# Kernel tuning notes

Measured on AMD Instinct MI355X. Metric: run time of the kernel, lower is better.

The kernel has to match this reference:

```python
import jax, jax.numpy as jnp
import numpy as np

N_ATOMS = 65536
N_SPECIES = 4
N_MOL = 512
F_PS = 512
F_MP = 256
H = 256
EPS = 1e-5


def _layer_norm(x, gamma, beta):
    mu = jnp.mean(x, axis=-1, keepdims=True)
    var = jnp.mean(jnp.square(x - mu), axis=-1, keepdims=True)
    return (x - mu) * jax.lax.rsqrt(var + EPS) * gamma + beta


def _species_mlp(x, W1, W2, W3):
    # x: [N, F], atoms grouped into S contiguous equal-size species blocks.
    S = W1.shape[0]
    N, F = x.shape
    xs = x.reshape(S, N // S, F)                       # [S, N/S, F]
    h = jax.nn.silu(jnp.einsum('snf,sfh->snh', xs, W1))  # grouped GEMM + SiLU
    h = jax.nn.silu(jnp.einsum('snh,sho->sno', h, W2))
    e = jnp.einsum('snh,sho->sno', h, W3)              # [S, N/S, 1]
    return e.reshape(N, -1)                            # keys_to_samples: back to per-atom


def setup_inputs() -> dict:
    key = jax.random.key(0)
    ks = jax.random.split(key, 10)
    inp = {
        'x_ps': jax.random.normal(ks[0], (N_ATOMS, F_PS), dtype=jnp.float32),
        'x_mp': jax.random.normal(ks[1], (N_ATOMS, F_MP), dtype=jnp.float32),
        'batch': jax.random.randint(ks[2], (N_ATOMS,), 0, N_MOL),
        'gamma_ps': jnp.ones((F_PS,), jnp.float32),
        'beta_ps': jnp.zeros((F_PS,), jnp.float32),
        'gamma_mp': jnp.ones((F_MP,), jnp.float32),
        'beta_mp': jnp.zeros((F_MP,), jnp.float32),
        'W_ps1': jax.random.normal(ks[3], (N_SPECIES, F_PS, H), jnp.float32) / np.sqrt(F_PS),
        'W_ps2': jax.random.normal(ks[4], (N_SPECIES, H, H), jnp.float32) / np.sqrt(H),
        'W_ps3': jax.random.normal(ks[5], (N_SPECIES, H, 1), jnp.float32) / np.sqrt(H),
        'W_mp1': jax.random.normal(ks[6], (N_SPECIES, F_MP, H), jnp.float32) / np.sqrt(F_MP),
        'W_mp2': jax.random.normal(ks[7], (N_SPECIES, H, H), jnp.float32) / np.sqrt(H),
        'W_mp3': jax.random.normal(ks[8], (N_SPECIES, H, 1), jnp.float32) / np.sqrt(H),
    }
    return inp


def reference(x_ps, x_mp, batch, gamma_ps, beta_ps, gamma_mp, beta_mp,
              W_ps1, W_ps2, W_ps3, W_mp1, W_mp2, W_mp3):
    norm_factor = jnp.float32(1.0)  # normalization_factor buffer
    f_ps = _layer_norm(x_ps, gamma_ps, beta_ps)
    f_mp = _layer_norm(x_mp, gamma_mp, beta_mp)
    e_ps = _species_mlp(f_ps, W_ps1, W_ps2, W_ps3)   # [N, 1] per-atom energies
    e_mp = _species_mlp(f_mp, W_mp1, W_mp2, W_mp3)   # [N, 1]
    # index_add_ scatter: per-atom -> per-molecule
    energies_ps = jax.ops.segment_sum(e_ps, batch, num_segments=N_MOL) / norm_factor
    energies_mp = jax.ops.segment_sum(e_mp, batch, num_segments=N_MOL) / norm_factor
    return energies_ps + energies_mp                 # [N_MOL, 1] (training path)
```

## Files before the change

kernel.cpp:

```cpp
#include <hip/hip_runtime.h>
#include <hip/hip_bf16.h>

#define N_ATOMS 65536
#define N_MOL 512

typedef __attribute__((ext_vector_type(8))) __bf16 bf16x8;
typedef __attribute__((ext_vector_type(4))) float f32x4;

__device__ __forceinline__ unsigned int f2bf(float f) {
    unsigned int u = __float_as_uint(f);
    return (u + 0x7fffu + ((u >> 16) & 1u)) >> 16;
}

__device__ __forceinline__ int pack2n(float a, float b) {
    union { __hip_bfloat162 h; int u; } c;
    c.h = __float22bfloat162_rn(make_float2(a, b));
    return c.u;
}

__device__ __forceinline__ short bf1(float a) {
    union { __hip_bfloat16 h; short s; } c;
    c.h = __float2bfloat16(a);
    return c.s;
}

__device__ __forceinline__ float silu(float v) {
    return v / (1.0f + __expf(-v));
}

#define GLDS16(gp, lp)                                                        \
    __builtin_amdgcn_global_load_lds(                                         \
        (__attribute__((address_space(1))) void*)(uintptr_t)(gp),             \
        (__attribute__((address_space(3))) void*)(uintptr_t)(lp), 16, 0, 0)

#define WS_W1PS 0
#define WS_W2PS 524288
#define WS_W1MP 786432
#define WS_W2MP 1048576
#define WS_GB_BYTES 2621440

__global__ __launch_bounds__(256) void prep_w(const float* __restrict__ Wps1,
                                              const float* __restrict__ Wps2,
                                              const float* __restrict__ Wmp1,
                                              const float* __restrict__ Wmp2,
                                              const float* __restrict__ g_ps,
                                              const float* __restrict__ b_ps,
                                              const float* __restrict__ g_mp,
                                              const float* __restrict__ b_mp,
                                              short* __restrict__ wdst,
                                              float* __restrict__ gb) {
    int b = blockIdx.x;
    const float* src; int K; long dstbase; int s, c;
    const float* ga = nullptr; const float* be = nullptr; float* gbd = nullptr;
    if (b < 32)      { src = Wps1; K = 512; s = b >> 3;        c = b & 7;        dstbase = WS_W1PS;
                       ga = g_ps; be = b_ps; gbd = gb; }
    else if (b < 48) { src = Wps2; K = 256; s = (b - 32) >> 2; c = (b - 32) & 3; dstbase = WS_W2PS; }
    else if (b < 64) { src = Wmp1; K = 256; s = (b - 48) >> 2; c = (b - 48) & 3; dstbase = WS_W1MP;
                       ga = g_mp; be = b_mp; gbd = gb + 2048; }
    else             { src = Wmp2; K = 256; s = (b - 64) >> 2; c = (b - 64) & 3; dstbase = WS_W2MP; }
    int n = threadIdx.x;
    int k0 = c * 64;
    const float* sp = src + (long)s * K * 256 + (long)k0 * 256 + n;
    int4* dstc = (int4*)(wdst + dstbase + (long)s * K * 256 + (long)c * 16384);
    float gs = 0.0f, bs = 0.0f;
    #pragma unroll 2
    for (int j = 0; j < 8; ++j) {
        unsigned int hh[8];
        #pragma unroll
        for (int i = 0; i < 8; ++i) {
            int kl = j * 8 + i;
            float v = sp[(long)kl * 256];
            float w = ga ? v * ga[k0 + kl] : v;
            hh[i] = f2bf(w);
            if (ga) {
                gs += __uint_as_float(hh[i] << 16);
                bs += be[k0 + kl] * v;
            }
        }
        int4 p;
        p.x = (int)(hh[0] | (hh[1] << 16));
        p.y = (int)(hh[2] | (hh[3] << 16));
        p.z = (int)(hh[4] | (hh[5] << 16));
        p.w = (int)(hh[6] | (hh[7] << 16));
        int ch = j >> 2;
        int i16 = n * 4 + ((j & 3) ^ ((n >> 1) & 3));
        dstc[ch * 1024 + i16] = p;
    }
    if (ga) {
        atomicAdd(&gbd[s * 256 + n], gs);
        atomicAdd(&gbd[1024 + s * 256 + n], bs);
    }
}

#define OFF_P0    0
#define OFF_AS    32768
#define OFF_H1    16384
#define OFF_STATS 49152
#define OFF_ELDS  49664
#define ARENA_BYTES 49920

#define STAGE_B(gbase, lbase)                                                 \
    do {                                                                      \
        const int4* _g = (const int4*)(gbase);                                \
        int4* _l = (int4*)(lbase);                                            \
        _Pragma("unroll")                                                     \
        for (int _q = 0; _q < 4; ++_q) {                                      \
            int _idx = wid * 256 + _q * 64;                                   \
            GLDS16(_g + _idx + lane, _l + _idx);                              \
        }                                                                     \
    } while (0)

template <int NPH>
__device__ __forceinline__ void mlp_body(
    char* arena,
    const float* __restrict__ x, const short* __restrict__ W1,
    const short* __restrict__ W2, const float* __restrict__ gW1,
    const float* __restrict__ bW1, const float* __restrict__ W3,
    const int* __restrict__ batch, float* __restrict__ out, int tile) {
    short* P0  = (short*)(arena + OFF_P0);
    short* As  = (short*)(arena + OFF_AS);
    short* H1  = (short*)(arena + OFF_H1);
    float2* rowstats = (float2*)(arena + OFF_STATS);
    float*  e_lds    = (float*)(arena + OFF_ELDS);

    const int tid = threadIdx.x;
    const int lane = tid & 63;
    const int wid = tid >> 6;
    const int wn = wid * 64;
    const int lg = lane >> 4;
    const int ln = lane & 15;
    const int swz = lg ^ ((ln >> 1) & 3);

    constexpr int F = NPH * 64;
    const int block0 = tile * 64;
    const int species = block0 >> 14;
    const short* W1s = W1 + (size_t)species * NPH * 16384;
    const short* W2s = W2 + (size_t)species * 65536;

    if (tid < 64) e_lds[tid] = 0.0f;
    const int mol = (tid < 64) ? batch[block0 + tid] : 0;

    float gwv[4], bwv[4], w3v[4];
    #pragma unroll
    for (int n = 0; n < 4; ++n) {
        int col = wn + n * 16 + ln;
        gwv[n] = gW1[species * 256 + col];
        bwv[n] = bW1[species * 256 + col];
        w3v[n] = W3[species * 256 + col];
    }

    const int ar = tid >> 2;
    const int aj = tid & 3;
    const float* xrow = x + (size_t)(block0 + ar) * F + aj * 8;
    const int i16a = ar * 4 + (aj ^ ((ar >> 1) & 3));

    f32x4 acc[4][4];
    #pragma unroll
    for (int m = 0; m < 4; ++m)
        #pragma unroll
        for (int n = 0; n < 4; ++n) acc[m][n] = (f32x4){0.f, 0.f, 0.f, 0.f};
    float s1 = 0.0f, s2 = 0.0f;

    float4 cu0 = *(const float4*)(xrow);
    float4 cv0 = *(const float4*)(xrow + 4);
    float4 cu1 = *(const float4*)(xrow + 32);
    float4 cv1 = *(const float4*)(xrow + 36);

    #pragma unroll 1
    for (int p = 0; p < NPH; ++p) {
        if (p) __syncthreads();
        float4 nu0, nv0, nu1, nv1;
        if (p + 1 < NPH) {
            nu0 = *(const float4*)(xrow + (p + 1) * 64);
            nv0 = *(const float4*)(xrow + (p + 1) * 64 + 4);
            nu1 = *(const float4*)(xrow + (p + 1) * 64 + 32);
            nv1 = *(const float4*)(xrow + (p + 1) * 64 + 36);
        }
        STAGE_B(W1s + (size_t)p * 16384, P0);
        STAGE_B(W1s + (size_t)p * 16384 + 8192, P0 + 8192);
        s1 += cu0.x + cu0.y + cu0.z + cu0.w + cv0.x + cv0.y + cv0.z + cv0.w
            + cu1.x + cu1.y + cu1.z + cu1.w + cv1.x + cv1.y + cv1.z + cv1.w;
        s2 += cu0.x * cu0.x + cu0.y * cu0.y + cu0.z * cu0.z + cu0.w * cu0.w
            + cv0.x * cv0.x + cv0.y * cv0.y + cv0.z * cv0.z + cv0.w * cv0.w
            + cu1.x * cu1.x + cu1.y * cu1.y + cu1.z * cu1.z + cu1.w * cu1.w
            + cv1.x * cv1.x + cv1.y * cv1.y + cv1.z * cv1.z + cv1.w * cv1.w;
        {
            int4 q;
            q.x = pack2n(cu0.x, cu0.y); q.y = pack2n(cu0.z, cu0.w);
            q.z = pack2n(cv0.x, cv0.y); q.w = pack2n(cv0.z, cv0.w);
            *(int4*)&As[i16a * 8] = q;
            q.x = pack2n(cu1.x, cu1.y); q.y = pack2n(cu1.z, cu1.w);
            q.z = pack2n(cv1.x, cv1.y); q.w = pack2n(cv1.z, cv1.w);
            *(int4*)&As[2048 + i16a * 8] = q;
        }
        __syncthreads();
        #pragma unroll
        for (int ks = 0; ks < 2; ++ks) {
            bf16x8 a[4], b[4];
            #pragma unroll
            for (int m = 0; m < 4; ++m)
                a[m] = *(const bf16x8*)&As[ks * 2048 + (m * 64 + ln * 4 + swz) * 8];
            #pragma unroll
            for (int n = 0; n < 4; ++n)
                b[n] = *(const bf16x8*)&P0[ks * 8192 + (wn * 4 + n * 64 + ln * 4 + swz) * 8];
            __builtin_amdgcn_s_setprio(1);
            #pragma unroll
            for (int m = 0; m < 4; ++m)
                #pragma unroll
                for (int n = 0; n < 4; ++n)
                    acc[m][n] = __builtin_amdgcn_mfma_f32_16x16x32_bf16(a[m], b[n], acc[m][n], 0, 0, 0);
            __builtin_amdgcn_s_setprio(0);
        }
        if (p + 1 < NPH) { cu0 = nu0; cv0 = nv0; cu1 = nu1; cv1 = nv1; }
    }

    s1 += __shfl_xor(s1, 1); s1 += __shfl_xor(s1, 2);
    s2 += __shfl_xor(s2, 1); s2 += __shfl_xor(s2, 2);
    if (aj == 0) rowstats[ar] = make_float2(s1, s2);
    __syncthreads();

    STAGE_B(W2s, P0);

    const float invF = 1.0f / (float)F;
    #pragma unroll
    for (int m = 0; m < 4; ++m) {
        #pragma unroll
        for (int rr = 0; rr < 4; ++rr) {
            int row = m * 16 + lg * 4 + rr;
            float2 rs = rowstats[row];
            float mu = rs.x * invF;
            float var = rs.y * invF - mu * mu;
            float rstd = rsqrtf(var + 1e-5f);
            float nmu = rstd * mu;
            #pragma unroll
            for (int n = 0; n < 4; ++n) {
                float vv = rstd * acc[m][n][rr] - nmu * gwv[n] + bwv[n];
                int col = wn + n * 16 + ln;
                H1[(row * 256 + col) ^ ((row & 7) << 3)] = bf1(silu(vv));
            }
        }
    }
    __syncthreads();

    f32x4 acc2[4][4];
    #pragma unroll
    for (int m = 0; m < 4; ++m)
        #pragma unroll
        for (int n = 0; n < 4; ++n) acc2[m][n] = (f32x4){0.f, 0.f, 0.f, 0.f};

    #pragma unroll 1
    for (int c = 0; c < 8; ++c) {
        bf16x8 a[4], b[4];
        #pragma unroll
        for (int m = 0; m < 4; ++m)
            a[m] = *(const bf16x8*)&H1[m * 4096 + ln * 256 + ((c * 32 + lg * 8) ^ ((ln & 7) << 3))];
        #pragma unroll
        for (int n = 0; n < 4; ++n)
            b[n] = *(const bf16x8*)&P0[(wn * 4 + n * 64 + ln * 4 + swz) * 8];
        __syncthreads();
        if (c < 7)
            STAGE_B(W2s + (size_t)(c + 1) * 8192, P0);
        __builtin_amdgcn_s_setprio(1);
        #pragma unroll
        for (int m = 0; m < 4; ++m)
            #pragma unroll
            for (int n = 0; n < 4; ++n)
                acc2[m][n] = __builtin_amdgcn_mfma_f32_16x16x32_bf16(a[m], b[n], acc2[m][n], 0, 0, 0);
        __builtin_amdgcn_s_setprio(0);
        __syncthreads();
    }

    #pragma unroll
    for (int m = 0; m < 4; ++m) {
        #pragma unroll
        for (int rr = 0; rr < 4; ++rr) {
            int row = m * 16 + lg * 4 + rr;
            float p = 0.0f;
            #pragma unroll
            for (int n = 0; n < 4; ++n) p += silu(acc2[m][n][rr]) * w3v[n];
            p += __shfl_xor(p, 1); p += __shfl_xor(p, 2);
            p += __shfl_xor(p, 4); p += __shfl_xor(p, 8);
            if (ln == 0) atomicAdd(&e_lds[row], p);
        }
    }
    __syncthreads();
    if (tid < 64) atomicAdd(out + mol, e_lds[tid]);
}

__global__ __launch_bounds__(256, 3) void mlp_all(
    const float* __restrict__ x_ps, const float* __restrict__ x_mp,
    const short* __restrict__ wimg, const float* __restrict__ gb,
    const float* __restrict__ W3ps, const float* __restrict__ W3mp,
    const int* __restrict__ batch, float* __restrict__ out) {
    __shared__ __align__(16) char arena[ARENA_BYTES];
    if (blockIdx.x < 1024) {
        mlp_body<8>(arena, x_ps, wimg + WS_W1PS, wimg + WS_W2PS,
                    gb + 0, gb + 1024, W3ps, batch, out, (int)blockIdx.x);
    } else {
        mlp_body<4>(arena, x_mp, wimg + WS_W1MP, wimg + WS_W2MP,
                    gb + 2048, gb + 3072, W3mp, batch, out, (int)blockIdx.x - 1024);
    }
}

extern "C" void kernel_launch(void* const* d_in, const int* in_sizes, int n_in,
                              void* d_out, int out_size, void* d_ws, size_t ws_size,
                              hipStream_t stream) {
    const float* x_ps     = (const float*)d_in[0];
    const float* x_mp     = (const float*)d_in[1];
    const int*   batch    = (const int*)d_in[2];
    const float* gamma_ps = (const float*)d_in[3];
    const float* beta_ps  = (const float*)d_in[4];
    const float* gamma_mp = (const float*)d_in[5];
    const float* beta_mp  = (const float*)d_in[6];
    const float* W_ps1    = (const float*)d_in[7];
    const float* W_ps2    = (const float*)d_in[8];
    const float* W_ps3    = (const float*)d_in[9];
    const float* W_mp1    = (const float*)d_in[10];
    const float* W_mp2    = (const float*)d_in[11];
    const float* W_mp3    = (const float*)d_in[12];

    float* out = (float*)d_out;
    short* wsW = (short*)d_ws;
    float* gb  = (float*)((char*)d_ws + WS_GB_BYTES);

    hipMemsetAsync(out, 0, N_MOL * sizeof(float), stream);
    hipMemsetAsync(gb, 0, 4096 * sizeof(float), stream);

    hipLaunchKernelGGL(prep_w, dim3(80), dim3(256), 0, stream,
                       W_ps1, W_ps2, W_mp1, W_mp2,
                       gamma_ps, beta_ps, gamma_mp, beta_mp, wsW, gb);

    hipLaunchKernelGGL(mlp_all, dim3(2048), dim3(256), 0, stream,
                       x_ps, x_mp, wsW, gb, W_ps3, W_mp3, batch, out);
}
```

Baseline: 151.0 us.

## Stage fp32 activations directly to LDS and prefetch next phase during MFMA

The input activation tile is now copied straight from global memory into LDS as fp32 with a swizzled layout. Previously it was loaded into registers, converted to bf16 and written to LDS by hand. Each phase reads all of its A and B fragments into registers, syncs, and then issues the next phase's W1 and X loads (or the W2 load on the last phase) before running the MFMAs, so the loads overlap compute. This trades more LDS read traffic, in-register bf16 conversion and larger register pressure for fewer VGPR round-trips and better latency hiding.

```diff
diff --git a/kernel.cpp b/kernel.cpp
--- a/kernel.cpp
+++ b/kernel.cpp
@@ -93,7 +93,7 @@
 }
 
 #define OFF_P0    0
-#define OFF_AS    32768
+#define OFF_XS    32768
 #define OFF_H1    16384
 #define OFF_STATS 49152
 #define OFF_ELDS  49664
@@ -110,6 +110,18 @@
         }                                                                     \
     } while (0)
 
+#define STAGE_X(p_)                                                           \
+    do {                                                                      \
+        _Pragma("unroll")                                                     \
+        for (int _q = 0; _q < 4; ++_q) {                                      \
+            int _u = wid * 256 + _q * 64 + lane;                              \
+            int _r = _u >> 4;                                                 \
+            int _j = (_u & 15) ^ (_r & 7);                                    \
+            const float* _g = x + (size_t)(block0 + _r) * F + (p_) * 64 + _j * 4; \
+            GLDS16(_g, Xs + (size_t)(wid * 256 + _q * 64) * 4);               \
+        }                                                                     \
+    } while (0)
+
 template <int NPH>
 __device__ __forceinline__ void mlp_body(
     char* arena,
@@ -118,7 +130,7 @@
     const float* __restrict__ bW1, const float* __restrict__ W3,
     const int* __restrict__ batch, float* __restrict__ out, int tile) {
     short* P0  = (short*)(arena + OFF_P0);
-    short* As  = (short*)(arena + OFF_AS);
+    float* Xs  = (float*)(arena + OFF_XS);
     short* H1  = (short*)(arena + OFF_H1);
     float2* rowstats = (float2*)(arena + OFF_STATS);
     float*  e_lds    = (float*)(arena + OFF_ELDS);
@@ -151,8 +163,6 @@
 
     const int ar = tid >> 2;
     const int aj = tid & 3;
-    const float* xrow = x + (size_t)(block0 + ar) * F + aj * 8;
-    const int i16a = ar * 4 + (aj ^ ((ar >> 1) & 3));
 
     f32x4 acc[4][4];
     #pragma unroll
@@ -161,65 +171,64 @@
         for (int n = 0; n < 4; ++n) acc[m][n] = (f32x4){0.f, 0.f, 0.f, 0.f};
     float s1 = 0.0f, s2 = 0.0f;
 
-    float4 cu0 = *(const float4*)(xrow);
-    float4 cv0 = *(const float4*)(xrow + 4);
-    float4 cu1 = *(const float4*)(xrow + 32);
-    float4 cv1 = *(const float4*)(xrow + 36);
+    STAGE_B(W1s, P0);
+    STAGE_B(W1s + 8192, P0 + 8192);
+    STAGE_X(0);
 
     #pragma unroll 1
     for (int p = 0; p < NPH; ++p) {
-        if (p) __syncthreads();
-        float4 nu0, nv0, nu1, nv1;
+        __syncthreads();
+        f32x4 st[4];
+        #pragma unroll
+        for (int i = 0; i < 4; ++i)
+            st[i] = *(const f32x4*)&Xs[(size_t)(ar * 16 + ((aj * 4 + i) ^ (ar & 7))) * 4];
+        bf16x8 afr[2][4], bfr[2][4];
+        #pragma unroll
+        for (int ks = 0; ks < 2; ++ks) {
+            #pragma unroll
+            for (int m = 0; m < 4; ++m) {
+                int row = m * 16 + ln;
+                int jl = ks * 8 + lg * 2;
+                f32x4 xa = *(const f32x4*)&Xs[(size_t)(row * 16 + ((jl    ) ^ (row & 7))) * 4];
+                f32x4 xb = *(const f32x4*)&Xs[(size_t)(row * 16 + ((jl + 1) ^ (row & 7))) * 4];
+                union { bf16x8 v; int4 q; } av;
+                av.q.x = pack2n(xa[0], xa[1]); av.q.y = pack2n(xa[2], xa[3]);
+                av.q.z = pack2n(xb[0], xb[1]); av.q.w = pack2n(xb[2], xb[3]);
+                afr[ks][m] = av.v;
+            }
+            #pragma unroll
+            for (int n = 0; n < 4; ++n)
+                bfr[ks][n] = *(const bf16x8*)&P0[ks * 8192 + (wn * 4 + n * 64 + ln * 4 + swz) * 8];
+        }
+        __syncthreads();
         if (p + 1 < NPH) {
-            nu0 = *(const float4*)(xrow + (p + 1) * 64);
-            nv0 = *(const float4*)(xrow + (p + 1) * 64 + 4);
-            nu1 = *(const float4*)(xrow + (p + 1) * 64 + 32);
-            nv1 = *(const float4*)(xrow + (p + 1) * 64 + 36);
-        }
-        STAGE_B(W1s + (size_t)p * 16384, P0);
-        STAGE_B(W1s + (size_t)p * 16384 + 8192, P0 + 8192);
-        s1 += cu0.x + cu0.y + cu0.z + cu0.w + cv0.x + cv0.y + cv0.z + cv0.w
-            + cu1.x + cu1.y + cu1.z + cu1.w + cv1.x + cv1.y + cv1.z + cv1.w;
-        s2 += cu0.x * cu0.x + cu0.y * cu0.y + cu0.z * cu0.z + cu0.w * cu0.w
-            + cv0.x * cv0.x + cv0.y * cv0.y + cv0.z * cv0.z + cv0.w * cv0.w
-            + cu1.x * cu1.x + cu1.y * cu1.y + cu1.z * cu1.z + cu1.w * cu1.w
-            + cv1.x * cv1.x + cv1.y * cv1.y + cv1.z * cv1.z + cv1.w * cv1.w;
-        {
-            int4 q;
-            q.x = pack2n(cu0.x, cu0.y); q.y = pack2n(cu0.z, cu0.w);
-            q.z = pack2n(cv0.x, cv0.y); q.w = pack2n(cv0.z, cv0.w);
-            *(int4*)&As[i16a * 8] = q;
-            q.x = pack2n(cu1.x, cu1.y); q.y = pack2n(cu1.z, cu1.w);
-            q.z = pack2n(cv1.x, cv1.y); q.w = pack2n(cv1.z, cv1.w);
-            *(int4*)&As[2048 + i16a * 8] = q;
-        }
-        __syncthreads();
-        #pragma unroll
-        for (int ks = 0; ks < 2; ++ks) {
-            bf16x8 a[4], b[4];
-            #pragma unroll
-            for (int m = 0; m < 4; ++m)
-                a[m] = *(const bf16x8*)&As[ks * 2048 + (m * 64 + ln * 4 + swz) * 8];
-            #pragma unroll
-            for (int n = 0; n < 4; ++n)
-                b[n] = *(const bf16x8*)&P0[ks * 8192 + (wn * 4 + n * 64 + ln * 4 + swz) * 8];
-            __builtin_amdgcn_s_setprio(1);
+            STAGE_B(W1s + (size_t)(p + 1) * 16384, P0);
+            STAGE_B(W1s + (size_t)(p + 1) * 16384 + 8192, P0 + 8192);
+            STAGE_X(p + 1);
+        } else {
+            STAGE_B(W2s, P0);
+        }
+        #pragma unroll
+        for (int i = 0; i < 4; ++i) {
+            s1 += st[i][0] + st[i][1] + st[i][2] + st[i][3];
+            s2 += st[i][0] * st[i][0] + st[i][1] * st[i][1]
+                + st[i][2] * st[i][2] + st[i][3] * st[i][3];
+        }
+        __builtin_amdgcn_s_setprio(1);
+        #pragma unroll
+        for (int ks = 0; ks < 2; ++ks)
             #pragma unroll
             for (int m = 0; m < 4; ++m)
                 #pragma unroll
                 for (int n = 0; n < 4; ++n)
-                    acc[m][n] = __builtin_amdgcn_mfma_f32_16x16x32_bf16(a[m], b[n], acc[m][n], 0, 0, 0);
-            __builtin_amdgcn_s_setprio(0);
-        }
-        if (p + 1 < NPH) { cu0 = nu0; cv0 = nv0; cu1 = nu1; cv1 = nv1; }
+                    acc[m][n] = __builtin_amdgcn_mfma_f32_16x16x32_bf16(afr[ks][m], bfr[ks][n], acc[m][n], 0, 0, 0);
+        __builtin_amdgcn_s_setprio(0);
     }
 
     s1 += __shfl_xor(s1, 1); s1 += __shfl_xor(s1, 2);
     s2 += __shfl_xor(s2, 1); s2 += __shfl_xor(s2, 2);
     if (aj == 0) rowstats[ar] = make_float2(s1, s2);
     __syncthreads();
-
-    STAGE_B(W2s, P0);
 
     const float invF = 1.0f / (float)F;
     #pragma unroll
```

Measured after the change: 400.2 us. 2.65x slower.
